# Performance work log

Measured on AMD Instinct MI355X. Metric: run time of the kernel, lower is better.

Reference implementation:

```python
import jax, jax.numpy as jnp
import numpy as np

C_M = 256
C = 32
C_Z = 128
EPS = 1e-5


def setup_inputs() -> dict:
    key = jax.random.key(0)
    ks = jax.random.split(key, 8)
    b, s, i = 1, 128, 256
    msa = jax.random.normal(ks[0], (b, s, i, C_M), dtype=jnp.float32)
    scale_in = 1.0 / np.sqrt(C_M)
    scale_out = 1.0 / np.sqrt(C * C)
    return {
        "msa_representation": msa,
        "ln_w": jnp.ones((C_M,), jnp.float32),
        "ln_b": jnp.zeros((C_M,), jnp.float32),
        "w_left": jax.random.normal(ks[1], (C_M, C), jnp.float32) * scale_in,
        "b_left": jax.random.normal(ks[2], (C,), jnp.float32) * scale_in,
        "w_right": jax.random.normal(ks[3], (C_M, C), jnp.float32) * scale_in,
        "b_right": jax.random.normal(ks[4], (C,), jnp.float32) * scale_in,
        "w_out": jax.random.normal(ks[5], (C * C, C_Z), jnp.float32) * scale_out,
        "b_out": jax.random.normal(ks[6], (C_Z,), jnp.float32) * scale_out,
    }


def reference(msa_representation, ln_w, ln_b, w_left, b_left, w_right, b_right, w_out, b_out):
    x = msa_representation
    # LayerNorm over c_m
    mu = jnp.mean(x, axis=-1, keepdims=True)
    var = jnp.mean(jnp.square(x - mu), axis=-1, keepdims=True)
    x = (x - mu) * jax.lax.rsqrt(var + EPS) * ln_w + ln_b
    # dual projections: [b, s, i, c]
    A = x @ w_left + b_left
    B = x @ w_right + b_right
    s_dim = x.shape[1]
    # outer product mean over MSA depth s: [b, i, j, c, c]
    outer = jnp.einsum('bsic,bsjd->bijcd', A, B) / s_dim
    b_, i_, j_ = outer.shape[0], outer.shape[1], outer.shape[2]
    flat = outer.reshape(b_, i_, j_, C * C)
    return flat @ w_out + b_out
```

## Files before the change

kernel.cpp:

```cpp
#include <hip/hip_runtime.h>

typedef __attribute__((ext_vector_type(8))) short short8;
typedef __attribute__((ext_vector_type(4))) float f32x4;

#define CM 256
#define CC 32
#define CZ 128
#define SDIM 128
#define IDIM 256

__device__ __forceinline__ unsigned short f2bf(float f) {
  union { float f; unsigned u; } v; v.f = f;
  unsigned r = v.u + 0x7fffu + ((v.u >> 16) & 1u);
  return (unsigned short)(r >> 16);
}

__global__ void k_prep(const float* __restrict__ wl, const float* __restrict__ wr,
                       const float* __restrict__ wo,
                       unsigned short* __restrict__ wlrT, unsigned short* __restrict__ WF) {
  int t = blockIdx.x * 256 + threadIdx.x;
  if (t < 64 * 256) {
    int c = t >> 8, e = t & 255;
    float v = (c < CC) ? wl[e * CC + c] : wr[e * CC + (c - CC)];
    wlrT[c * 256 + e] = f2bf(v);
  } else {
    int t2 = t - 64 * 256;
    if (t2 < 8 * 32 * 64) {
      int zt = t2 >> 11, ks = (t2 >> 6) & 31, lane = t2 & 63;
      int ln = lane & 15, qd = lane >> 4;
      int z = zt * 16 + ln;
#pragma unroll
      for (int e = 0; e < 8; ++e) {
        int c = qd * 8 + e, d = ks;
        WF[(size_t)t2 * 8 + e] = f2bf(wo[(c * 32 + d) * CZ + z] * (1.0f / 128.0f));
      }
    }
  }
}

__global__ __launch_bounds__(512) void k_lnproj(
    const float* __restrict__ x, const float* __restrict__ lnw, const float* __restrict__ lnb,
    const float* __restrict__ bl, const float* __restrict__ br,
    const unsigned short* __restrict__ wlrT,
    unsigned short* __restrict__ A2, unsigned short* __restrict__ Bbuf) {
  extern __shared__ __align__(16) char lds[];
  unsigned short* xn = (unsigned short*)lds;
  unsigned short* sT = (unsigned short*)(lds + 67584);
  int tid = threadIdx.x;
  int lane = tid & 63, ww = tid >> 6;
  int qd = lane >> 4, ln = lane & 15;
  int i = blockIdx.x;

  for (int rr = 0; rr < 16; ++rr) {
    int s = ww * 16 + rr;
    float4 v = ((const float4*)(x + ((size_t)s * IDIM + i) * CM))[lane];
    float s1 = v.x + v.y + v.z + v.w;
    float s2 = v.x * v.x + v.y * v.y + v.z * v.z + v.w * v.w;
#pragma unroll
    for (int off = 32; off; off >>= 1) {
      s1 += __shfl_xor(s1, off);
      s2 += __shfl_xor(s2, off);
    }
    float mu = s1 * (1.0f / 256.0f);
    float var = s2 * (1.0f / 256.0f) - mu * mu;
    float rs = rsqrtf(var + 1e-5f);
    float4 w4 = ((const float4*)lnw)[lane];
    float4 b4 = ((const float4*)lnb)[lane];
    ushort4 h;
    h.x = f2bf((v.x - mu) * rs * w4.x + b4.x);
    h.y = f2bf((v.y - mu) * rs * w4.y + b4.y);
    h.z = f2bf((v.z - mu) * rs * w4.z + b4.z);
    h.w = f2bf((v.w - mu) * rs * w4.w + b4.w);
    *(ushort4*)&xn[s * 264 + lane * 4] = h;
  }
  __syncthreads();

  f32x4 acc[4];
#pragma unroll
  for (int nt = 0; nt < 4; ++nt) acc[nt] = (f32x4){0.f, 0.f, 0.f, 0.f};
#pragma unroll
  for (int ks = 0; ks < 8; ++ks) {
    short8 af = *(const short8*)&xn[(ww * 16 + ln) * 264 + ks * 32 + qd * 8];
#pragma unroll
    for (int nt = 0; nt < 4; ++nt) {
      short8 bf = *(const short8*)(wlrT + (nt * 16 + ln) * 256 + ks * 32 + qd * 8);
      acc[nt] = __builtin_amdgcn_mfma_f32_16x16x32_bf16(af, bf, acc[nt], 0, 0, 0);
    }
  }
#pragma unroll
  for (int nt = 0; nt < 4; ++nt) {
    int c64 = nt * 16 + ln;
    float bias = (c64 < CC) ? bl[c64] : br[c64 - CC];
    ushort4 h;
    h.x = f2bf(acc[nt][0] + bias);
    h.y = f2bf(acc[nt][1] + bias);
    h.z = f2bf(acc[nt][2] + bias);
    h.w = f2bf(acc[nt][3] + bias);
    *(ushort4*)&sT[c64 * 136 + ww * 16 + qd * 4] = h;
  }
  __syncthreads();

  {
    int rtloc = ww >> 2, ks4 = ww & 3;
    short8 v = *(const short8*)&sT[(rtloc * 16 + ln) * 136 + ks4 * 32 + qd * 8];
    *(short8*)(A2 + ((size_t)(((2 * i + rtloc) * 4 + ks4) * 64 + lane)) * 8) = v;
  }
  {
    int row = tid >> 4, ch = tid & 15;
    short8 v = *(const short8*)&sT[(CC + row) * 136 + ch * 8];
    *(short8*)(Bbuf + ((size_t)(i * CC + row)) * SDIM + ch * 8) = v;
  }
}

__global__ __launch_bounds__(512, 4) void k_main(
    const unsigned short* __restrict__ A2, const unsigned short* __restrict__ Bbuf,
    const unsigned short* __restrict__ WF, const float* __restrict__ bout,
    float* __restrict__ out) {
  extern __shared__ __align__(16) char lds[];
  unsigned short* sB = (unsigned short*)lds;
  unsigned short* sP = (unsigned short*)lds;
  float* redF = (float*)lds;
  int tid = threadIdx.x;
  int lane = tid & 63, ww = tid >> 6;
  int qd = lane >> 4, ln = lane & 15;
  int i0 = blockIdx.x * 8, j0 = blockIdx.y * 4;

#pragma unroll
  for (int t = 0; t < 4; ++t) {
    int idx = tid + t * 512;
    int r = idx >> 4, ch = idx & 15;
    short8 v = *(const short8*)(Bbuf + (size_t)(j0 * CC + r) * SDIM + ch * 8);
    *(short8*)&sB[r * 136 + ch * 8] = v;
  }
  __syncthreads();

  int wy = ww >> 1, wx = ww & 1;
  f32x4 acc1[4][4];
#pragma unroll
  for (int a = 0; a < 4; ++a)
#pragma unroll
    for (int b = 0; b < 4; ++b) acc1[a][b] = (f32x4){0.f, 0.f, 0.f, 0.f};
#pragma unroll
  for (int ks = 0; ks < 4; ++ks) {
    short8 af[4];
#pragma unroll
    for (int ti = 0; ti < 4; ++ti)
      af[ti] = *(const short8*)(A2 + ((size_t)((i0 * 2 + wy * 4 + ti) * 4 + ks) * 64 + lane) * 8);
#pragma unroll
    for (int tj = 0; tj < 4; ++tj) {
      short8 bf = *(const short8*)&sB[(wx * 64 + tj * 16 + ln) * 136 + ks * 32 + qd * 8];
#pragma unroll
      for (int ti = 0; ti < 4; ++ti)
        acc1[ti][tj] = __builtin_amdgcn_mfma_f32_16x16x32_bf16(af[ti], bf, acc1[ti][tj], 0, 0, 0);
    }
  }

  f32x4 acc2[2][4];
#pragma unroll
  for (int mt = 0; mt < 2; ++mt)
#pragma unroll
    for (int z4 = 0; z4 < 4; ++z4) acc2[mt][z4] = (f32x4){0.f, 0.f, 0.f, 0.f};

  for (int h = 0; h < 2; ++h) {
    __syncthreads();
#pragma unroll
    for (int ti = 0; ti < 4; ++ti) {
      int iloc = 2 * wy + (ti >> 1);
      int cbase = 16 * (ti & 1) + qd * 4;
      int cb = cbase >> 3;
#pragma unroll
      for (int u = 0; u < 2; ++u) {
        int tj = h + u * 2;
        int jloc = 2 * wx + (tj >> 1);
        int p = iloc * 4 + jloc;
        ushort4 hh;
        hh.x = f2bf(acc1[ti][tj][0]);
        hh.y = f2bf(acc1[ti][tj][1]);
        hh.z = f2bf(acc1[ti][tj][2]);
        hh.w = f2bf(acc1[ti][tj][3]);
        *(ushort4*)&sP[p * 520 + ln * 32 + ((((ln >> 1) & 3) ^ cb) * 8) + (cbase & 7)] = hh;
      }
    }
    __syncthreads();
    if (ww < 4) {
      int zth = ww & 1, kq = ww >> 1;
#pragma unroll
      for (int kk = 0; kk < 8; ++kk) {
        int ksp = kq * 8 + kk;
        int gks = h * 16 + ksp;
        short8 afr[2];
#pragma unroll
        for (int mt = 0; mt < 2; ++mt)
          afr[mt] = *(const short8*)&sP[(mt * 16 + ln) * 520 + ksp * 32 + ((((ksp >> 1) & 3) ^ qd) * 8)];
#pragma unroll
        for (int z4 = 0; z4 < 4; ++z4) {
          int zt = zth * 4 + z4;
          short8 bfr = *(const short8*)(WF + ((size_t)(zt * 32 + gks) * 64 + lane) * 8);
#pragma unroll
          for (int mt = 0; mt < 2; ++mt)
            acc2[mt][z4] = __builtin_amdgcn_mfma_f32_16x16x32_bf16(afr[mt], bfr, acc2[mt][z4], 0, 0, 0);
        }
      }
    }
  }

  __syncthreads();
  if (ww == 2 || ww == 3) {
    int zth = ww & 1;
#pragma unroll
    for (int mt = 0; mt < 2; ++mt)
#pragma unroll
      for (int z4 = 0; z4 < 4; ++z4)
#pragma unroll
        for (int rg = 0; rg < 4; ++rg) {
          int p = mt * 16 + qd * 4 + rg;
          redF[(zth * 32 + p) * 68 + z4 * 16 + ln] = acc2[mt][z4][rg];
        }
  }
  __syncthreads();
  if (ww == 0 || ww == 1) {
    int zth = ww & 1;
#pragma unroll
    for (int mt = 0; mt < 2; ++mt)
#pragma unroll
      for (int z4 = 0; z4 < 4; ++z4) {
        int z = (zth * 4 + z4) * 16 + ln;
        float bz = bout[z];
#pragma unroll
        for (int rg = 0; rg < 4; ++rg) {
          int p = mt * 16 + qd * 4 + rg;
          float v = acc2[mt][z4][rg] + redF[(zth * 32 + p) * 68 + z4 * 16 + ln] + bz;
          out[((size_t)(i0 + (p >> 2)) * IDIM + (j0 + (p & 3))) * CZ + z] = v;
        }
      }
  }
}

extern "C" void kernel_launch(void* const* d_in, const int* in_sizes, int n_in,
                              void* d_out, int out_size, void* d_ws, size_t ws_size,
                              hipStream_t stream) {
  const float* msa = (const float*)d_in[0];
  const float* lnw = (const float*)d_in[1];
  const float* lnb = (const float*)d_in[2];
  const float* wl  = (const float*)d_in[3];
  const float* bl  = (const float*)d_in[4];
  const float* wr  = (const float*)d_in[5];
  const float* br  = (const float*)d_in[6];
  const float* wo  = (const float*)d_in[7];
  const float* bo  = (const float*)d_in[8];
  float* out = (float*)d_out;

  char* ws = (char*)d_ws;
  unsigned short* A2   = (unsigned short*)ws;
  unsigned short* Bbuf = (unsigned short*)(ws + (2u << 20));
  unsigned short* wlrT = (unsigned short*)(ws + (4u << 20));
  unsigned short* WF   = (unsigned short*)(ws + (4u << 20) + 32768);

  (void)hipFuncSetAttribute((const void*)k_lnproj,
                            hipFuncAttributeMaxDynamicSharedMemorySize, 84992);

  k_prep<<<128, 256, 0, stream>>>(wl, wr, wo, wlrT, WF);
  k_lnproj<<<256, 512, 84992, stream>>>(msa, lnw, lnb, bl, br, wlrT, A2, Bbuf);
  k_main<<<dim3(32, 64), 512, 34816, stream>>>(A2, Bbuf, WF, bo, out);
}
```

Before: 152.2 us.

## Enlarge k_main tile to 8x8 pairs with 1024-thread blocks and single-pass projection

The main kernel now handles an 8x8 (i,j) tile per block with 16 waves instead of 8x4 with 8 waves, halving the grid. Each WF weight fragment is reused across twice as many output rows, and the two-half staging loop for the outer-product tile is replaced by one staging pass into a larger LDS buffer. The split-K reduction becomes a two-level tree, output stores are vectorised as float4, and the bf16 packing uses a cheaper round-half-up conversion. The cost is much more LDS per block (about 129 KB), lower occupancy, and half the waves sitting idle during the second GEMM.

```diff
diff --git a/kernel.cpp b/kernel.cpp
--- a/kernel.cpp
+++ b/kernel.cpp
@@ -13,6 +13,10 @@
   union { float f; unsigned u; } v; v.f = f;
   unsigned r = v.u + 0x7fffu + ((v.u >> 16) & 1u);
   return (unsigned short)(r >> 16);
+}
+__device__ __forceinline__ unsigned pack_bf2(float a, float b) {
+  union { float f; unsigned u; } x, y; x.f = a; y.f = b;
+  return ((x.u + 0x8000u) >> 16) | ((y.u + 0x8000u) & 0xffff0000u);
 }
 
 __global__ void k_prep(const float* __restrict__ wl, const float* __restrict__ wr,
@@ -112,7 +116,7 @@
   }
 }
 
-__global__ __launch_bounds__(512, 4) void k_main(
+__global__ __launch_bounds__(1024) void k_main(
     const unsigned short* __restrict__ A2, const unsigned short* __restrict__ Bbuf,
     const unsigned short* __restrict__ WF, const float* __restrict__ bout,
     float* __restrict__ out) {
@@ -123,18 +127,18 @@
   int tid = threadIdx.x;
   int lane = tid & 63, ww = tid >> 6;
   int qd = lane >> 4, ln = lane & 15;
-  int i0 = blockIdx.x * 8, j0 = blockIdx.y * 4;
+  int i0 = blockIdx.x * 8, j0 = blockIdx.y * 8;
 
 #pragma unroll
   for (int t = 0; t < 4; ++t) {
-    int idx = tid + t * 512;
+    int idx = tid + t * 1024;
     int r = idx >> 4, ch = idx & 15;
     short8 v = *(const short8*)(Bbuf + (size_t)(j0 * CC + r) * SDIM + ch * 8);
     *(short8*)&sB[r * 136 + ch * 8] = v;
   }
   __syncthreads();
 
-  int wy = ww >> 1, wx = ww & 1;
+  int wy = ww >> 2, wx = ww & 3;
   f32x4 acc1[4][4];
 #pragma unroll
   for (int a = 0; a < 4; ++a)
@@ -154,85 +158,91 @@
         acc1[ti][tj] = __builtin_amdgcn_mfma_f32_16x16x32_bf16(af[ti], bf, acc1[ti][tj], 0, 0, 0);
     }
   }
-
-  f32x4 acc2[2][4];
-#pragma unroll
-  for (int mt = 0; mt < 2; ++mt)
-#pragma unroll
-    for (int z4 = 0; z4 < 4; ++z4) acc2[mt][z4] = (f32x4){0.f, 0.f, 0.f, 0.f};
-
-  for (int h = 0; h < 2; ++h) {
-    __syncthreads();
-#pragma unroll
-    for (int ti = 0; ti < 4; ++ti) {
-      int iloc = 2 * wy + (ti >> 1);
-      int cbase = 16 * (ti & 1) + qd * 4;
-      int cb = cbase >> 3;
-#pragma unroll
-      for (int u = 0; u < 2; ++u) {
-        int tj = h + u * 2;
-        int jloc = 2 * wx + (tj >> 1);
-        int p = iloc * 4 + jloc;
-        ushort4 hh;
-        hh.x = f2bf(acc1[ti][tj][0]);
-        hh.y = f2bf(acc1[ti][tj][1]);
-        hh.z = f2bf(acc1[ti][tj][2]);
-        hh.w = f2bf(acc1[ti][tj][3]);
-        *(ushort4*)&sP[p * 520 + ln * 32 + ((((ln >> 1) & 3) ^ cb) * 8) + (cbase & 7)] = hh;
+  __syncthreads();
+
+#pragma unroll
+  for (int ti = 0; ti < 4; ++ti) {
+    int iloc = wy * 2 + (ti >> 1);
+    int cbase = 16 * (ti & 1) + qd * 4;
+    int cb = cbase >> 3;
+#pragma unroll
+    for (int tj = 0; tj < 4; ++tj) {
+      int jloc = wx * 2 + (tj >> 1);
+      int d = 16 * (tj & 1) + ln;
+      int p = iloc * 8 + jloc;
+      uint2 u;
+      u.x = pack_bf2(acc1[ti][tj][0], acc1[ti][tj][1]);
+      u.y = pack_bf2(acc1[ti][tj][2], acc1[ti][tj][3]);
+      *(uint2*)&sP[p * 1032 + d * 32 + ((((d >> 1) & 3) ^ cb) * 8) + (cbase & 7)] = u;
+    }
+  }
+  __syncthreads();
+
+  int ztq = ww & 1, kq = ww >> 1;
+  f32x4 acc2[4][4];
+#pragma unroll
+  for (int a = 0; a < 4; ++a)
+#pragma unroll
+    for (int b = 0; b < 4; ++b) acc2[a][b] = (f32x4){0.f, 0.f, 0.f, 0.f};
+  if (ww < 8) {
+#pragma unroll
+    for (int cc = 0; cc < 8; ++cc) {
+      int ks = kq * 8 + cc;
+      short8 afr[4];
+#pragma unroll
+      for (int mt = 0; mt < 4; ++mt)
+        afr[mt] = *(const short8*)&sP[(mt * 16 + ln) * 1032 + ks * 32 + ((((ks >> 1) & 3) ^ qd) * 8)];
+#pragma unroll
+      for (int z4 = 0; z4 < 4; ++z4) {
+        int zt = ztq * 4 + z4;
+        short8 bfr = *(const short8*)(WF + ((size_t)(zt * 32 + ks) * 64 + lane) * 8);
+#pragma unroll
+        for (int mt = 0; mt < 4; ++mt)
+          acc2[z4][mt] = __builtin_amdgcn_mfma_f32_16x16x32_bf16(bfr, afr[mt], acc2[z4][mt], 0, 0, 0);
       }
     }
-    __syncthreads();
-    if (ww < 4) {
-      int zth = ww & 1, kq = ww >> 1;
-#pragma unroll
-      for (int kk = 0; kk < 8; ++kk) {
-        int ksp = kq * 8 + kk;
-        int gks = h * 16 + ksp;
-        short8 afr[2];
-#pragma unroll
-        for (int mt = 0; mt < 2; ++mt)
-          afr[mt] = *(const short8*)&sP[(mt * 16 + ln) * 520 + ksp * 32 + ((((ksp >> 1) & 3) ^ qd) * 8)];
-#pragma unroll
-        for (int z4 = 0; z4 < 4; ++z4) {
-          int zt = zth * 4 + z4;
-          short8 bfr = *(const short8*)(WF + ((size_t)(zt * 32 + gks) * 64 + lane) * 8);
-#pragma unroll
-          for (int mt = 0; mt < 2; ++mt)
-            acc2[mt][z4] = __builtin_amdgcn_mfma_f32_16x16x32_bf16(afr[mt], bfr, acc2[mt][z4], 0, 0, 0);
-        }
+  }
+
+  __syncthreads();
+  if (ww < 8 && kq >= 2) {
+    int s = (kq - 2) * 2 + ztq;
+#pragma unroll
+    for (int z4 = 0; z4 < 4; ++z4)
+#pragma unroll
+      for (int mt = 0; mt < 4; ++mt)
+        *(f32x4*)&redF[(s * 64 + mt * 16 + ln) * 68 + z4 * 16 + qd * 4] = acc2[z4][mt];
+  }
+  __syncthreads();
+  if (ww < 8 && kq < 2) {
+    int s = kq * 2 + ztq;
+#pragma unroll
+    for (int z4 = 0; z4 < 4; ++z4)
+#pragma unroll
+      for (int mt = 0; mt < 4; ++mt)
+        acc2[z4][mt] += *(const f32x4*)&redF[(s * 64 + mt * 16 + ln) * 68 + z4 * 16 + qd * 4];
+  }
+  __syncthreads();
+  if (ww < 8 && kq == 1) {
+#pragma unroll
+    for (int z4 = 0; z4 < 4; ++z4)
+#pragma unroll
+      for (int mt = 0; mt < 4; ++mt)
+        *(f32x4*)&redF[(ztq * 64 + mt * 16 + ln) * 68 + z4 * 16 + qd * 4] = acc2[z4][mt];
+  }
+  __syncthreads();
+  if (ww < 8 && kq == 0) {
+#pragma unroll
+    for (int z4 = 0; z4 < 4; ++z4) {
+      int z = (ztq * 4 + z4) * 16 + qd * 4;
+      f32x4 bz = *(const f32x4*)(bout + z);
+#pragma unroll
+      for (int mt = 0; mt < 4; ++mt) {
+        int p = mt * 16 + ln;
+        f32x4 v = acc2[z4][mt] + *(const f32x4*)&redF[(ztq * 64 + p) * 68 + z4 * 16 + qd * 4] + bz;
+        int i = i0 + (p >> 3), j = j0 + (p & 7);
+        *(f32x4*)&out[((size_t)i * IDIM + j) * CZ + z] = v;
       }
     }
-  }
-
-  __syncthreads();
-  if (ww == 2 || ww == 3) {
-    int zth = ww & 1;
-#pragma unroll
-    for (int mt = 0; mt < 2; ++mt)
-#pragma unroll
-      for (int z4 = 0; z4 < 4; ++z4)
-#pragma unroll
-        for (int rg = 0; rg < 4; ++rg) {
-          int p = mt * 16 + qd * 4 + rg;
-          redF[(zth * 32 + p) * 68 + z4 * 16 + ln] = acc2[mt][z4][rg];
-        }
-  }
-  __syncthreads();
-  if (ww == 0 || ww == 1) {
-    int zth = ww & 1;
-#pragma unroll
-    for (int mt = 0; mt < 2; ++mt)
-#pragma unroll
-      for (int z4 = 0; z4 < 4; ++z4) {
-        int z = (zth * 4 + z4) * 16 + ln;
-        float bz = bout[z];
-#pragma unroll
-        for (int rg = 0; rg < 4; ++rg) {
-          int p = mt * 16 + qd * 4 + rg;
-          float v = acc2[mt][z4][rg] + redF[(zth * 32 + p) * 68 + z4 * 16 + ln] + bz;
-          out[((size_t)(i0 + (p >> 2)) * IDIM + (j0 + (p & 3))) * CZ + z] = v;
-        }
-      }
   }
 }
 
@@ -258,8 +268,10 @@
 
   (void)hipFuncSetAttribute((const void*)k_lnproj,
                             hipFuncAttributeMaxDynamicSharedMemorySize, 84992);
+  (void)hipFuncSetAttribute((const void*)k_main,
+                            hipFuncAttributeMaxDynamicSharedMemorySize, 132096);
 
   k_prep<<<128, 256, 0, stream>>>(wl, wr, wo, wlrT, WF);
   k_lnproj<<<256, 512, 84992, stream>>>(msa, lnw, lnb, bl, br, wlrT, A2, Bbuf);
-  k_main<<<dim3(32, 64), 512, 34816, stream>>>(A2, Bbuf, WF, bo, out);
-}
+  k_main<<<dim3(32, 32), 1024, 132096, stream>>>(A2, Bbuf, WF, bo, out);
+}
```

New measurement: 157.2 us. 3.3% more time.
